# Kernel optimization log

Measured on AMD Instinct MI355X. Metric: run time of the kernel, lower is better.

## Reference

```python
import jax, jax.numpy as jnp
import numpy as np
from jax import lax


def haar_dwt2(x):
    """Level-1 Haar (db1) 2D DWT on [N, H, W] with even H, W.
    Returns cA, cH, cV (cD is discarded by the module), each [N, H//2, W//2].
    Matches pywt/ptwt db1 block form: cA=(a+b+c+d)/2, etc."""
    a = x[:, 0::2, 0::2]
    b = x[:, 0::2, 1::2]
    c = x[:, 1::2, 0::2]
    d = x[:, 1::2, 1::2]
    cA = (a + b + c + d) * 0.5
    cH = (a + b - c - d) * 0.5  # horizontal detail (highpass along rows axis)
    cV = (a - b + c - d) * 0.5  # vertical detail (highpass along cols axis)
    return cA, cH, cV


def conv2d_same(x, w, b):
    # x: [N, Cin, H, W], w: [Cout, Cin, kh, kw]
    y = lax.conv_general_dilated(x, w, window_strides=(1, 1), padding='SAME',
                                 dimension_numbers=('NCHW', 'OIHW', 'NCHW'))
    return y + b[None, :, None, None]


def maxpool2(x):
    return lax.reduce_window(x, -jnp.inf, lax.max,
                             window_dimensions=(1, 1, 2, 2),
                             window_strides=(1, 1, 2, 2), padding='VALID')


def setup_inputs() -> dict:
    key = jax.random.key(0)
    ks = jax.random.split(key, 7)
    B, C, H, W = 32, 3, 512, 512
    x = jax.random.normal(ks[0], (B, C, H, W), dtype=jnp.float32)
    # conv stack params (Conv2d(1,16,3), Conv2d(16,8,3), Conv2d(8,4,1))
    w1 = jax.random.normal(ks[1], (16, 1, 3, 3), dtype=jnp.float32) * (1.0 / 3.0)
    b1 = jnp.zeros((16,), dtype=jnp.float32)
    w2 = jax.random.normal(ks[2], (8, 16, 3, 3), dtype=jnp.float32) * (1.0 / 12.0)
    b2 = jnp.zeros((8,), dtype=jnp.float32)
    w3 = jax.random.normal(ks[3], (4, 8, 1, 1), dtype=jnp.float32) * (1.0 / 2.83)
    b3 = jnp.zeros((4,), dtype=jnp.float32)
    return {"x": x, "w1": w1, "b1": b1, "w2": w2, "b2": b2, "w3": w3, "b3": b3}


def reference(x, w1, b1, w2, b2, w3, b3):
    B, C, H, W = x.shape
    # Batch the per-image/per-channel loop: treat each channel as one map.
    flat = x.reshape(B * C, H, W)
    cA, cH, cV = haar_dwt2(flat)  # [B*C, H/2, W/2]

    # Low-frequency conv stack on approx coeffs (1 input channel per map).
    h = cA[:, None, :, :]                       # [B*C, 1, H/2, W/2]
    h = maxpool2(jax.nn.relu(conv2d_same(h, w1, b1)))
    h = maxpool2(jax.nn.relu(conv2d_same(h, w2, b2)))
    h = conv2d_same(h, w3, b3)                  # [B*C, 4, H/8, W/8]
    # per-channel flatten, then concat over channels (dim=1 in the original)
    low = h.reshape(B, 1, -1)                   # [B, 1, C*4*(H/8)*(W/8)]

    # High-frequency: per channel concat [cH.flatten(), cV.flatten()],
    # then concat over channels.
    n = (H // 2) * (W // 2)
    high = jnp.concatenate([cH.reshape(B, C, n), cV.reshape(B, C, n)], axis=-1)
    high = high.reshape(B, 1, C * 2 * n)        # [B, 1, C*2*(H/2)*(W/2)]
    return low, high
```

## Files before the change

### kernel.cpp

```cpp
#include <hip/hip_runtime.h>


typedef float v2f __attribute__((ext_vector_type(2)));

#define PK_FMA_W0(acc, w, d) \
    asm("v_pk_fma_f32 %0, %1, %2, %0 op_sel:[0,0,0] op_sel_hi:[1,0,1]" \
        : "+v"(acc) : "s"(w), "v"(d))
#define PK_FMA_W1(acc, w, d) \
    asm("v_pk_fma_f32 %0, %1, %2, %0 op_sel:[0,1,0] op_sel_hi:[1,1,1]" \
        : "+v"(acc) : "s"(w), "v"(d))
#define PK_MUL_W0(dst, w, d) \
    asm("v_pk_mul_f32 %0, %1, %2 op_sel:[0,0] op_sel_hi:[1,0]" \
        : "=v"(dst) : "s"(w), "v"(d))
#define PK_MUL_W1(dst, w, d) \
    asm("v_pk_mul_f32 %0, %1, %2 op_sel:[0,1] op_sel_hi:[1,1]" \
        : "=v"(dst) : "s"(w), "v"(d))

__global__ __launch_bounds__(256, 8) void fused_all_kernel(
    const float* __restrict__ x,
    const float* __restrict__ w1, const float* __restrict__ b1,
    const float* __restrict__ w2, const float* __restrict__ b2,
    const float* __restrict__ w3, const float* __restrict__ b3,
    float* __restrict__ outLow, float* __restrict__ outHigh)
{
    __shared__ __align__(16) float ca[22 * 70];
    __shared__ __align__(16) float h1s[4 * 10 * 34];

    int wvi = threadIdx.x >> 6;
    int lni = threadIdx.x & 63;

    int pos = threadIdx.x & 63;
    int ocg = __builtin_amdgcn_readfirstlane(wvi);
    int ly = pos >> 4, lx = pos & 15;

    #pragma unroll 1
    for (int j3 = 0; j3 < 3; ++j3) {
        int tIdx = blockIdx.x * 3 + j3;
        int img  = tIdx >> 6;
        int s    = tIdx & 63;
        int rs = s >> 2, cs = s & 3;
        int hy0 = rs * 8 - 1, hx0 = cs * 32 - 1;
        int cy0 = rs * 16 - 3, cx0 = cs * 64 - 3;

        const float* xi = x + img * 262144;
        float* hb = outHigh + img * 131072;

        {
            int i = threadIdx.x;
            int row = i >> 4, cg = i & 15;
            int gy = rs * 16 + row;
            int gx = cs * 64 + cg * 4;
            const float* r0 = xi + (2 * gy) * 512 + 2 * gx;
            const float* r1 = r0 + 512;
            float4 t0 = *(const float4*)(r0);
            float4 t1 = *(const float4*)(r0 + 4);
            float4 u0 = *(const float4*)(r1);
            float4 u1 = *(const float4*)(r1 + 4);
            float4 vA, vH, vV;
            vA.x = (t0.x + t0.y + u0.x + u0.y) * 0.5f;
            vH.x = (t0.x + t0.y - u0.x - u0.y) * 0.5f;
            vV.x = (t0.x - t0.y + u0.x - u0.y) * 0.5f;
            vA.y = (t0.z + t0.w + u0.z + u0.w) * 0.5f;
            vH.y = (t0.z + t0.w - u0.z - u0.w) * 0.5f;
            vV.y = (t0.z - t0.w + u0.z - u0.w) * 0.5f;
            vA.z = (t1.x + t1.y + u1.x + u1.y) * 0.5f;
            vH.z = (t1.x + t1.y - u1.x - u1.y) * 0.5f;
            vV.z = (t1.x - t1.y + u1.x - u1.y) * 0.5f;
            vA.w = (t1.z + t1.w + u1.z + u1.w) * 0.5f;
            vH.w = (t1.z + t1.w - u1.z - u1.w) * 0.5f;
            vV.w = (t1.z - t1.w + u1.z - u1.w) * 0.5f;
            int po = (gy << 8) + gx;
            *(float4*)(hb + po) = vH;
            *(float4*)(hb + 65536 + po) = vV;
            float* cp = ca + (row + 3) * 70 + cg * 4 + 3;
            cp[0] = vA.x; cp[1] = vA.y; cp[2] = vA.z; cp[3] = vA.w;
        }

        #pragma unroll
        for (int j = 0; j < 3; ++j) {
            if (j < 2 || lni < 1) {
                int i = wvi * 129 + j * 64 + lni;
                int r, c;
                if (i < 210)      { r = i / 70;              c = i - r * 70; }
                else if (i < 420) { int jj = i - 210; r = 19 + jj / 70; c = jj - (jj / 70) * 70; }
                else              { int jj = i - 420; r = 3 + jj / 6; int k6 = jj - (jj / 6) * 6;
                                    c = (k6 < 3) ? k6 : (64 + k6); }
                int gy = cy0 + r, gx = cx0 + c;
                float v = 0.f;
                if ((unsigned)gy < 256u && (unsigned)gx < 256u) {
                    const float* p0 = xi + (2 * gy) * 512 + 2 * gx;
                    float2 a = *(const float2*)(p0);
                    float2 b = *(const float2*)(p0 + 512);
                    v = (a.x + a.y + b.x + b.y) * 0.5f;
                }
                ca[r * 70 + c] = v;
            }
        }

        v2f acc2[2][2];
        #pragma unroll
        for (int r = 0; r < 2; ++r)
            #pragma unroll
            for (int c = 0; c < 2; ++c) acc2[r][c] = (v2f){0.f, 0.f};

        __syncthreads();

        #pragma unroll 1
        for (int cc = 0; cc < 4; ++cc) {
            v2f wp1[2][9];
            #pragma unroll
            for (int o2 = 0; o2 < 2; ++o2)
                #pragma unroll
                for (int k = 0; k < 9; ++k)
                    wp1[o2][k] = (v2f){ w1[(cc * 4 + o2 * 2    ) * 9 + k],
                                        w1[(cc * 4 + o2 * 2 + 1) * 9 + k] };
            if (cc) __syncthreads();

            #pragma unroll 1
            for (int j = 0; j < 2; ++j) {
                if (j < 1 || lni < 21) {
                    int i = wvi * 85 + j * 64 + lni;
                    int hy = i / 34, hx = i - hy * 34;
                    const float* pb = ca + (2 * hy) * 70 + 2 * hx;
                    v2f pr[4][2];
                    #pragma unroll
                    for (int r = 0; r < 4; ++r) {
                        pr[r][0] = *(const v2f*)(pb + r * 70);
                        pr[r][1] = *(const v2f*)(pb + r * 70 + 2);
                    }
                    bool oob = ((unsigned)(hy0 + hy) >= 128u) | ((unsigned)(hx0 + hx) >= 128u);
                    v2f am[2][4];
                    #pragma unroll
                    for (int ky = 0; ky < 3; ++ky)
                    #pragma unroll
                    for (int kx = 0; kx < 3; ++kx) {
                        #pragma unroll
                        for (int o2 = 0; o2 < 2; ++o2)
                        #pragma unroll
                        for (int dy = 0; dy < 2; ++dy)
                        #pragma unroll
                        for (int dx = 0; dx < 2; ++dx) {
                            v2f d = pr[ky + dy][(kx + dx) >> 1];
                            if (ky == 0 && kx == 0) {
                                if (((kx + dx) & 1) == 0) PK_MUL_W0(am[o2][dy * 2 + dx], wp1[o2][0], d);
                                else                      PK_MUL_W1(am[o2][dy * 2 + dx], wp1[o2][0], d);
                            } else {
                                if (((kx + dx) & 1) == 0) PK_FMA_W0(am[o2][dy * 2 + dx], wp1[o2][ky * 3 + kx], d);
                                else                      PK_FMA_W1(am[o2][dy * 2 + dx], wp1[o2][ky * 3 + kx], d);
                            }
                        }
                    }
                    #pragma unroll
                    for (int o2 = 0; o2 < 2; ++o2) {
                        float mx = fmaxf(fmaxf(am[o2][0].x, am[o2][1].x),
                                         fmaxf(am[o2][2].x, am[o2][3].x));
                        float my = fmaxf(fmaxf(am[o2][0].y, am[o2][1].y),
                                         fmaxf(am[o2][2].y, am[o2][3].y));
                        mx = fmaxf(mx + b1[cc * 4 + o2 * 2    ], 0.f);
                        my = fmaxf(my + b1[cc * 4 + o2 * 2 + 1], 0.f);
                        h1s[((o2 * 2    ) * 10 + hy) * 34 + hx] = oob ? 0.f : mx;
                        h1s[((o2 * 2 + 1) * 10 + hy) * 34 + hx] = oob ? 0.f : my;
                    }
                }
            }
            __syncthreads();

            #pragma unroll
            for (int icl = 0; icl < 4; ++icl) {
                int ic = cc * 4 + icl;
                v2f wl[9];
                {
                    int oc0 = ocg * 2;
                    #pragma unroll
                    for (int k = 0; k < 9; ++k)
                        wl[k] = (v2f){ w2[((oc0    ) * 16 + ic) * 9 + k],
                                       w2[((oc0 + 1) * 16 + ic) * 9 + k] };
                }
                const float* base = h1s + (icl * 10 + ly * 2) * 34 + lx * 2;
                v2f wr[4][2];
                #pragma unroll
                for (int r = 0; r < 4; ++r) {
                    wr[r][0] = *(const v2f*)(base + r * 34);
                    wr[r][1] = *(const v2f*)(base + r * 34 + 2);
                }
                #pragma unroll
                for (int ky = 0; ky < 3; ++ky)
                #pragma unroll
                for (int kx = 0; kx < 3; ++kx) {
                    #pragma unroll
                    for (int r = 0; r < 2; ++r)
                    #pragma unroll
                    for (int c = 0; c < 2; ++c) {
                        v2f d = wr[r + ky][(c + kx) >> 1];
                        if (((c + kx) & 1) == 0) PK_FMA_W0(acc2[r][c], wl[ky * 3 + kx], d);
                        else                     PK_FMA_W1(acc2[r][c], wl[ky * 3 + kx], d);
                    }
                }
            }
        }

        float h2a, h2b;
        {
            float mx = fmaxf(fmaxf(acc2[0][0].x, acc2[0][1].x),
                             fmaxf(acc2[1][0].x, acc2[1][1].x));
            float my = fmaxf(fmaxf(acc2[0][0].y, acc2[0][1].y),
                             fmaxf(acc2[1][0].y, acc2[1][1].y));
            h2a = fmaxf(mx + b2[ocg * 2    ], 0.f);
            h2b = fmaxf(my + b2[ocg * 2 + 1], 0.f);
        }
        __syncthreads();
        float* hx2 = h1s;
        hx2[pos * 9 + ocg * 2    ] = h2a;
        hx2[pos * 9 + ocg * 2 + 1] = h2b;
        __syncthreads();

        float hv[8];
        #pragma unroll
        for (int ic = 0; ic < 8; ++ic) hv[ic] = hx2[pos * 9 + ic];
        float* dst = outLow + img * 16384;
        int posg = (rs * 4 + ly) * 64 + cs * 16 + lx;
        int oc3 = ocg;
        float sacc = b3[oc3];
        #pragma unroll
        for (int ic = 0; ic < 8; ++ic) sacc += w3[oc3 * 8 + ic] * hv[ic];
        dst[oc3 * 4096 + posg] = sacc;
    }
}

extern "C" void kernel_launch(void* const* d_in, const int* in_sizes, int n_in,
                              void* d_out, int out_size, void* d_ws, size_t ws_size,
                              hipStream_t stream) {
    const float* x  = (const float*)d_in[0];
    const float* w1 = (const float*)d_in[1];
    const float* b1 = (const float*)d_in[2];
    const float* w2 = (const float*)d_in[3];
    const float* b2 = (const float*)d_in[4];
    const float* w3 = (const float*)d_in[5];
    const float* b3 = (const float*)d_in[6];
    float* out     = (float*)d_out;
    float* outLow  = out;
    float* outHigh = out + 1572864;

    fused_all_kernel<<<2048, 256, 0, stream>>>(x, w1, b1, w2, b2, w3, b3,
                                               outLow, outHigh);
}
```

Baseline: 231.4 us.

## Double tile height per block and drop the per-block three-tile loop

Each block now covers a 32x64 cA tile with 512 threads, one tile per block, where before it covered 16x64 tiles with 256 threads and looped over three of them. The taller tile shares its halo rows over more output, so less redundant halo Haar and conv1 work is done, and the per-block tile loop is gone. In exchange, shared memory and block size grow, which may lower occupancy. The last conv1 pass now runs only 100 of 512 threads, leaving many lanes idle.

```diff
diff --git a/kernel.cpp b/kernel.cpp
--- a/kernel.cpp
+++ b/kernel.cpp
@@ -16,215 +16,205 @@
     asm("v_pk_mul_f32 %0, %1, %2 op_sel:[0,1] op_sel_hi:[1,1]" \
         : "=v"(dst) : "s"(w), "v"(d))
 
-__global__ __launch_bounds__(256, 8) void fused_all_kernel(
+__global__ __launch_bounds__(512, 8) void fused_all_kernel(
     const float* __restrict__ x,
     const float* __restrict__ w1, const float* __restrict__ b1,
     const float* __restrict__ w2, const float* __restrict__ b2,
     const float* __restrict__ w3, const float* __restrict__ b3,
     float* __restrict__ outLow, float* __restrict__ outHigh)
 {
-    __shared__ __align__(16) float ca[22 * 70];
-    __shared__ __align__(16) float h1s[4 * 10 * 34];
-
-    int wvi = threadIdx.x >> 6;
-    int lni = threadIdx.x & 63;
-
-    int pos = threadIdx.x & 63;
-    int ocg = __builtin_amdgcn_readfirstlane(wvi);
+    __shared__ __align__(16) float ca[38 * 70];
+    __shared__ __align__(16) float h1s[4 * 18 * 34];
+
+    int tid = threadIdx.x;
+
+    int tIdx = blockIdx.x;
+    int img  = tIdx >> 5;
+    int t    = tIdx & 31;
+    int tyy = t >> 2, txx = t & 3;
+    int hy0 = tyy * 16 - 1, hx0 = txx * 32 - 1;
+    int cy0 = tyy * 32 - 3, cx0 = txx * 64 - 3;
+
+    const float* xi = x + img * 262144;
+    float* hb = outHigh + img * 131072;
+
+    {
+        int i = tid;
+        int row = i >> 4, cg = i & 15;
+        int gy = tyy * 32 + row;
+        int gx = txx * 64 + cg * 4;
+        const float* r0 = xi + (2 * gy) * 512 + 2 * gx;
+        const float* r1 = r0 + 512;
+        float4 t0 = *(const float4*)(r0);
+        float4 t1 = *(const float4*)(r0 + 4);
+        float4 u0 = *(const float4*)(r1);
+        float4 u1 = *(const float4*)(r1 + 4);
+        float4 vA, vH, vV;
+        vA.x = (t0.x + t0.y + u0.x + u0.y) * 0.5f;
+        vH.x = (t0.x + t0.y - u0.x - u0.y) * 0.5f;
+        vV.x = (t0.x - t0.y + u0.x - u0.y) * 0.5f;
+        vA.y = (t0.z + t0.w + u0.z + u0.w) * 0.5f;
+        vH.y = (t0.z + t0.w - u0.z - u0.w) * 0.5f;
+        vV.y = (t0.z - t0.w + u0.z - u0.w) * 0.5f;
+        vA.z = (t1.x + t1.y + u1.x + u1.y) * 0.5f;
+        vH.z = (t1.x + t1.y - u1.x - u1.y) * 0.5f;
+        vV.z = (t1.x - t1.y + u1.x - u1.y) * 0.5f;
+        vA.w = (t1.z + t1.w + u1.z + u1.w) * 0.5f;
+        vH.w = (t1.z + t1.w - u1.z - u1.w) * 0.5f;
+        vV.w = (t1.z - t1.w + u1.z - u1.w) * 0.5f;
+        int po = (gy << 8) + gx;
+        *(float4*)(hb + po) = vH;
+        *(float4*)(hb + 65536 + po) = vV;
+        float* cp = ca + (row + 3) * 70 + cg * 4 + 3;
+        cp[0] = vA.x; cp[1] = vA.y; cp[2] = vA.z; cp[3] = vA.w;
+    }
+
+    #pragma unroll 1
+    for (int i = tid; i < 612; i += 512) {
+        int r, c;
+        if (i < 210)      { r = i / 70;              c = i - r * 70; }
+        else if (i < 420) { int j = i - 210; r = 35 + j / 70; c = j - (j / 70) * 70; }
+        else              { int j = i - 420; r = 3 + j / 6; int k6 = j - (j / 6) * 6;
+                            c = (k6 < 3) ? k6 : (64 + k6); }
+        int gy = cy0 + r, gx = cx0 + c;
+        float v = 0.f;
+        if ((unsigned)gy < 256u && (unsigned)gx < 256u) {
+            const float* p0 = xi + (2 * gy) * 512 + 2 * gx;
+            float2 a = *(const float2*)(p0);
+            float2 b = *(const float2*)(p0 + 512);
+            v = (a.x + a.y + b.x + b.y) * 0.5f;
+        }
+        ca[r * 70 + c] = v;
+    }
+
+    int pos = tid & 127;
+    int ocg = __builtin_amdgcn_readfirstlane(tid >> 7);
     int ly = pos >> 4, lx = pos & 15;
 
+    v2f acc2[2][2];
+    #pragma unroll
+    for (int r = 0; r < 2; ++r)
+        #pragma unroll
+        for (int c = 0; c < 2; ++c) acc2[r][c] = (v2f){0.f, 0.f};
+
+    __syncthreads();
+
     #pragma unroll 1
-    for (int j3 = 0; j3 < 3; ++j3) {
-        int tIdx = blockIdx.x * 3 + j3;
-        int img  = tIdx >> 6;
-        int s    = tIdx & 63;
-        int rs = s >> 2, cs = s & 3;
-        int hy0 = rs * 8 - 1, hx0 = cs * 32 - 1;
-        int cy0 = rs * 16 - 3, cx0 = cs * 64 - 3;
-
-        const float* xi = x + img * 262144;
-        float* hb = outHigh + img * 131072;
-
-        {
-            int i = threadIdx.x;
-            int row = i >> 4, cg = i & 15;
-            int gy = rs * 16 + row;
-            int gx = cs * 64 + cg * 4;
-            const float* r0 = xi + (2 * gy) * 512 + 2 * gx;
-            const float* r1 = r0 + 512;
-            float4 t0 = *(const float4*)(r0);
-            float4 t1 = *(const float4*)(r0 + 4);
-            float4 u0 = *(const float4*)(r1);
-            float4 u1 = *(const float4*)(r1 + 4);
-            float4 vA, vH, vV;
-            vA.x = (t0.x + t0.y + u0.x + u0.y) * 0.5f;
-            vH.x = (t0.x + t0.y - u0.x - u0.y) * 0.5f;
-            vV.x = (t0.x - t0.y + u0.x - u0.y) * 0.5f;
-            vA.y = (t0.z + t0.w + u0.z + u0.w) * 0.5f;
-            vH.y = (t0.z + t0.w - u0.z - u0.w) * 0.5f;
-            vV.y = (t0.z - t0.w + u0.z - u0.w) * 0.5f;
-            vA.z = (t1.x + t1.y + u1.x + u1.y) * 0.5f;
-            vH.z = (t1.x + t1.y - u1.x - u1.y) * 0.5f;
-            vV.z = (t1.x - t1.y + u1.x - u1.y) * 0.5f;
-            vA.w = (t1.z + t1.w + u1.z + u1.w) * 0.5f;
-            vH.w = (t1.z + t1.w - u1.z - u1.w) * 0.5f;
-            vV.w = (t1.z - t1.w + u1.z - u1.w) * 0.5f;
-            int po = (gy << 8) + gx;
-            *(float4*)(hb + po) = vH;
-            *(float4*)(hb + 65536 + po) = vV;
-            float* cp = ca + (row + 3) * 70 + cg * 4 + 3;
-            cp[0] = vA.x; cp[1] = vA.y; cp[2] = vA.z; cp[3] = vA.w;
-        }
-
+    for (int cc = 0; cc < 4; ++cc) {
+        v2f wp1[2][9];
         #pragma unroll
-        for (int j = 0; j < 3; ++j) {
-            if (j < 2 || lni < 1) {
-                int i = wvi * 129 + j * 64 + lni;
-                int r, c;
-                if (i < 210)      { r = i / 70;              c = i - r * 70; }
-                else if (i < 420) { int jj = i - 210; r = 19 + jj / 70; c = jj - (jj / 70) * 70; }
-                else              { int jj = i - 420; r = 3 + jj / 6; int k6 = jj - (jj / 6) * 6;
-                                    c = (k6 < 3) ? k6 : (64 + k6); }
-                int gy = cy0 + r, gx = cx0 + c;
-                float v = 0.f;
-                if ((unsigned)gy < 256u && (unsigned)gx < 256u) {
-                    const float* p0 = xi + (2 * gy) * 512 + 2 * gx;
-                    float2 a = *(const float2*)(p0);
-                    float2 b = *(const float2*)(p0 + 512);
-                    v = (a.x + a.y + b.x + b.y) * 0.5f;
-                }
-                ca[r * 70 + c] = v;
-            }
-        }
-
-        v2f acc2[2][2];
-        #pragma unroll
-        for (int r = 0; r < 2; ++r)
-            #pragma unroll
-            for (int c = 0; c < 2; ++c) acc2[r][c] = (v2f){0.f, 0.f};
-
-        __syncthreads();
+        for (int o2 = 0; o2 < 2; ++o2)
+            #pragma unroll
+            for (int k = 0; k < 9; ++k)
+                wp1[o2][k] = (v2f){ w1[(cc * 4 + o2 * 2    ) * 9 + k],
+                                    w1[(cc * 4 + o2 * 2 + 1) * 9 + k] };
+        if (cc) __syncthreads();
 
         #pragma unroll 1
-        for (int cc = 0; cc < 4; ++cc) {
-            v2f wp1[2][9];
-            #pragma unroll
-            for (int o2 = 0; o2 < 2; ++o2)
-                #pragma unroll
-                for (int k = 0; k < 9; ++k)
-                    wp1[o2][k] = (v2f){ w1[(cc * 4 + o2 * 2    ) * 9 + k],
-                                        w1[(cc * 4 + o2 * 2 + 1) * 9 + k] };
-            if (cc) __syncthreads();
-
-            #pragma unroll 1
-            for (int j = 0; j < 2; ++j) {
-                if (j < 1 || lni < 21) {
-                    int i = wvi * 85 + j * 64 + lni;
-                    int hy = i / 34, hx = i - hy * 34;
-                    const float* pb = ca + (2 * hy) * 70 + 2 * hx;
-                    v2f pr[4][2];
-                    #pragma unroll
-                    for (int r = 0; r < 4; ++r) {
-                        pr[r][0] = *(const v2f*)(pb + r * 70);
-                        pr[r][1] = *(const v2f*)(pb + r * 70 + 2);
-                    }
-                    bool oob = ((unsigned)(hy0 + hy) >= 128u) | ((unsigned)(hx0 + hx) >= 128u);
-                    v2f am[2][4];
-                    #pragma unroll
-                    for (int ky = 0; ky < 3; ++ky)
-                    #pragma unroll
-                    for (int kx = 0; kx < 3; ++kx) {
-                        #pragma unroll
-                        for (int o2 = 0; o2 < 2; ++o2)
-                        #pragma unroll
-                        for (int dy = 0; dy < 2; ++dy)
-                        #pragma unroll
-                        for (int dx = 0; dx < 2; ++dx) {
-                            v2f d = pr[ky + dy][(kx + dx) >> 1];
-                            if (ky == 0 && kx == 0) {
-                                if (((kx + dx) & 1) == 0) PK_MUL_W0(am[o2][dy * 2 + dx], wp1[o2][0], d);
-                                else                      PK_MUL_W1(am[o2][dy * 2 + dx], wp1[o2][0], d);
-                            } else {
-                                if (((kx + dx) & 1) == 0) PK_FMA_W0(am[o2][dy * 2 + dx], wp1[o2][ky * 3 + kx], d);
-                                else                      PK_FMA_W1(am[o2][dy * 2 + dx], wp1[o2][ky * 3 + kx], d);
-                            }
-                        }
-                    }
-                    #pragma unroll
-                    for (int o2 = 0; o2 < 2; ++o2) {
-                        float mx = fmaxf(fmaxf(am[o2][0].x, am[o2][1].x),
-                                         fmaxf(am[o2][2].x, am[o2][3].x));
-                        float my = fmaxf(fmaxf(am[o2][0].y, am[o2][1].y),
-                                         fmaxf(am[o2][2].y, am[o2][3].y));
-                        mx = fmaxf(mx + b1[cc * 4 + o2 * 2    ], 0.f);
-                        my = fmaxf(my + b1[cc * 4 + o2 * 2 + 1], 0.f);
-                        h1s[((o2 * 2    ) * 10 + hy) * 34 + hx] = oob ? 0.f : mx;
-                        h1s[((o2 * 2 + 1) * 10 + hy) * 34 + hx] = oob ? 0.f : my;
+        for (int i = tid; i < 612; i += 512) {
+            int hy = i / 34, hx = i - hy * 34;
+            const float* pb = ca + (2 * hy) * 70 + 2 * hx;
+            v2f pr[4][2];
+            #pragma unroll
+            for (int r = 0; r < 4; ++r) {
+                pr[r][0] = *(const v2f*)(pb + r * 70);
+                pr[r][1] = *(const v2f*)(pb + r * 70 + 2);
+            }
+            bool oob = ((unsigned)(hy0 + hy) >= 128u) | ((unsigned)(hx0 + hx) >= 128u);
+            v2f am[2][4];
+            #pragma unroll
+            for (int ky = 0; ky < 3; ++ky)
+            #pragma unroll
+            for (int kx = 0; kx < 3; ++kx) {
+                #pragma unroll
+                for (int o2 = 0; o2 < 2; ++o2)
+                #pragma unroll
+                for (int dy = 0; dy < 2; ++dy)
+                #pragma unroll
+                for (int dx = 0; dx < 2; ++dx) {
+                    v2f d = pr[ky + dy][(kx + dx) >> 1];
+                    if (ky == 0 && kx == 0) {
+                        if (((kx + dx) & 1) == 0) PK_MUL_W0(am[o2][dy * 2 + dx], wp1[o2][0], d);
+                        else                      PK_MUL_W1(am[o2][dy * 2 + dx], wp1[o2][0], d);
+                    } else {
+                        if (((kx + dx) & 1) == 0) PK_FMA_W0(am[o2][dy * 2 + dx], wp1[o2][ky * 3 + kx], d);
+                        else                      PK_FMA_W1(am[o2][dy * 2 + dx], wp1[o2][ky * 3 + kx], d);
                     }
                 }
             }
-            __syncthreads();
-
-            #pragma unroll
-            for (int icl = 0; icl < 4; ++icl) {
-                int ic = cc * 4 + icl;
-                v2f wl[9];
-                {
-                    int oc0 = ocg * 2;
-                    #pragma unroll
-                    for (int k = 0; k < 9; ++k)
-                        wl[k] = (v2f){ w2[((oc0    ) * 16 + ic) * 9 + k],
-                                       w2[((oc0 + 1) * 16 + ic) * 9 + k] };
-                }
-                const float* base = h1s + (icl * 10 + ly * 2) * 34 + lx * 2;
-                v2f wr[4][2];
-                #pragma unroll
-                for (int r = 0; r < 4; ++r) {
-                    wr[r][0] = *(const v2f*)(base + r * 34);
-                    wr[r][1] = *(const v2f*)(base + r * 34 + 2);
-                }
-                #pragma unroll
-                for (int ky = 0; ky < 3; ++ky)
-                #pragma unroll
-                for (int kx = 0; kx < 3; ++kx) {
-                    #pragma unroll
-                    for (int r = 0; r < 2; ++r)
-                    #pragma unroll
-                    for (int c = 0; c < 2; ++c) {
-                        v2f d = wr[r + ky][(c + kx) >> 1];
-                        if (((c + kx) & 1) == 0) PK_FMA_W0(acc2[r][c], wl[ky * 3 + kx], d);
-                        else                     PK_FMA_W1(acc2[r][c], wl[ky * 3 + kx], d);
-                    }
-                }
-            }
-        }
-
-        float h2a, h2b;
-        {
-            float mx = fmaxf(fmaxf(acc2[0][0].x, acc2[0][1].x),
-                             fmaxf(acc2[1][0].x, acc2[1][1].x));
-            float my = fmaxf(fmaxf(acc2[0][0].y, acc2[0][1].y),
-                             fmaxf(acc2[1][0].y, acc2[1][1].y));
-            h2a = fmaxf(mx + b2[ocg * 2    ], 0.f);
-            h2b = fmaxf(my + b2[ocg * 2 + 1], 0.f);
+            #pragma unroll
+            for (int o2 = 0; o2 < 2; ++o2) {
+                float mx = fmaxf(fmaxf(am[o2][0].x, am[o2][1].x),
+                                 fmaxf(am[o2][2].x, am[o2][3].x));
+                float my = fmaxf(fmaxf(am[o2][0].y, am[o2][1].y),
+                                 fmaxf(am[o2][2].y, am[o2][3].y));
+                mx = fmaxf(mx + b1[cc * 4 + o2 * 2    ], 0.f);
+                my = fmaxf(my + b1[cc * 4 + o2 * 2 + 1], 0.f);
+                h1s[((o2 * 2    ) * 18 + hy) * 34 + hx] = oob ? 0.f : mx;
+                h1s[((o2 * 2 + 1) * 18 + hy) * 34 + hx] = oob ? 0.f : my;
+            }
         }
         __syncthreads();
-        float* hx2 = h1s;
-        hx2[pos * 9 + ocg * 2    ] = h2a;
-        hx2[pos * 9 + ocg * 2 + 1] = h2b;
-        __syncthreads();
-
-        float hv[8];
+
         #pragma unroll
-        for (int ic = 0; ic < 8; ++ic) hv[ic] = hx2[pos * 9 + ic];
-        float* dst = outLow + img * 16384;
-        int posg = (rs * 4 + ly) * 64 + cs * 16 + lx;
-        int oc3 = ocg;
-        float sacc = b3[oc3];
-        #pragma unroll
-        for (int ic = 0; ic < 8; ++ic) sacc += w3[oc3 * 8 + ic] * hv[ic];
-        dst[oc3 * 4096 + posg] = sacc;
-    }
+        for (int icl = 0; icl < 4; ++icl) {
+            int ic = cc * 4 + icl;
+            v2f wl[9];
+            {
+                int oc0 = ocg * 2;
+                #pragma unroll
+                for (int k = 0; k < 9; ++k)
+                    wl[k] = (v2f){ w2[((oc0    ) * 16 + ic) * 9 + k],
+                                   w2[((oc0 + 1) * 16 + ic) * 9 + k] };
+            }
+            const float* base = h1s + (icl * 18 + ly * 2) * 34 + lx * 2;
+            v2f wr[4][2];
+            #pragma unroll
+            for (int r = 0; r < 4; ++r) {
+                wr[r][0] = *(const v2f*)(base + r * 34);
+                wr[r][1] = *(const v2f*)(base + r * 34 + 2);
+            }
+            #pragma unroll
+            for (int ky = 0; ky < 3; ++ky)
+            #pragma unroll
+            for (int kx = 0; kx < 3; ++kx) {
+                #pragma unroll
+                for (int r = 0; r < 2; ++r)
+                #pragma unroll
+                for (int c = 0; c < 2; ++c) {
+                    v2f d = wr[r + ky][(c + kx) >> 1];
+                    if (((c + kx) & 1) == 0) PK_FMA_W0(acc2[r][c], wl[ky * 3 + kx], d);
+                    else                     PK_FMA_W1(acc2[r][c], wl[ky * 3 + kx], d);
+                }
+            }
+        }
+    }
+
+    float h2a, h2b;
+    {
+        float mx = fmaxf(fmaxf(acc2[0][0].x, acc2[0][1].x),
+                         fmaxf(acc2[1][0].x, acc2[1][1].x));
+        float my = fmaxf(fmaxf(acc2[0][0].y, acc2[0][1].y),
+                         fmaxf(acc2[1][0].y, acc2[1][1].y));
+        h2a = fmaxf(mx + b2[ocg * 2    ], 0.f);
+        h2b = fmaxf(my + b2[ocg * 2 + 1], 0.f);
+    }
+    __syncthreads();
+    float* hx2 = h1s;
+    hx2[pos * 9 + ocg * 2    ] = h2a;
+    hx2[pos * 9 + ocg * 2 + 1] = h2b;
+    __syncthreads();
+
+    float hv[8];
+    #pragma unroll
+    for (int ic = 0; ic < 8; ++ic) hv[ic] = hx2[pos * 9 + ic];
+    float* dst = outLow + img * 16384;
+    int posg = (tyy * 8 + ly) * 64 + txx * 16 + lx;
+    int oc3 = ocg;
+    float sacc = b3[oc3];
+    #pragma unroll
+    for (int ic = 0; ic < 8; ++ic) sacc += w3[oc3 * 8 + ic] * hv[ic];
+    dst[oc3 * 4096 + posg] = sacc;
 }
 
 extern "C" void kernel_launch(void* const* d_in, const int* in_sizes, int n_in,
@@ -241,6 +231,6 @@
     float* outLow  = out;
     float* outHigh = out + 1572864;
 
-    fused_all_kernel<<<2048, 256, 0, stream>>>(x, w1, b1, w2, b2, w3, b3,
+    fused_all_kernel<<<3072, 512, 0, stream>>>(x, w1, b1, w2, b2, w3, b3,
                                                outLow, outHigh);
 }
```

After: 205.1 us. -11.4%, faster.
